# Optimization experiments

Hardware: AMD Instinct MI355X
Metric: run time of the kernel (lower is better)

Reference implementation:

```python
import jax, jax.numpy as jnp
import numpy as np

N = 20000      # nodes
E = 320000     # edges (avg degree 16)
D = 128        # emb_dim
L = 5          # num_layer
NV = 119       # node vocab (atom types)
EV = 5         # edge vocab (bond types)
BN_EPS = 1e-5


def setup_inputs() -> dict:
    key = jax.random.key(0)
    ks = jax.random.split(key, 8)
    s = 0.1
    return {
        "x": jax.random.randint(ks[0], (N,), 0, NV),
        "edge_index": jax.random.randint(ks[1], (2, E), 0, N),
        "edge_attr": jax.random.randint(ks[2], (E,), 0, EV),
        "node_emb1": jax.random.normal(ks[3], (NV, D), jnp.float32) * s,
        "node_emb2": jax.random.normal(ks[4], (NV, D), jnp.float32) * s,
        "edge_emb": jax.random.normal(ks[5], (2, L, EV, D), jnp.float32) * s,
        "eps": jnp.zeros((2, L), jnp.float32),
        "W": jax.random.normal(ks[6], (2, L, D, D), jnp.float32) / np.sqrt(D).astype(np.float32),
        "b": jnp.zeros((2, L, D), jnp.float32),
        "bn_gamma": jnp.ones((2, L, D), jnp.float32),
        "bn_beta": jnp.zeros((2, L, D), jnp.float32),
        "cross_unit": jnp.full((L, 2, 2), 0.5, jnp.float32),
    }


def gin_conv(h, src, dst, eattr, edge_tab, eps, W, b):
    # message: relu(x_j + edge_embedding), aggregated by add at target nodes
    msg = jax.nn.relu(h[src] + edge_tab[eattr])            # [E, D]
    agg = jax.ops.segment_sum(msg, dst, num_segments=h.shape[0])  # [N, D]
    return ((1.0 + eps) * h + agg) @ W.T + b               # mlp = single Linear


def batch_norm(h, gamma, beta):
    # training-mode BatchNorm1d over the node dimension (biased variance)
    mu = h.mean(axis=0)
    var = h.var(axis=0)
    return (h - mu) * jax.lax.rsqrt(var + BN_EPS) * gamma + beta


def reference(x, edge_index, edge_attr, node_emb1, node_emb2, edge_emb, eps, W, b,
              bn_gamma, bn_beta, cross_unit):
    src, dst = edge_index[0], edge_index[1]
    h1 = node_emb1[x]   # NodeEncoder tower 1
    h2 = node_emb2[x]   # NodeEncoder tower 2
    for l in range(L):
        a1 = gin_conv(h1, src, dst, edge_attr, edge_emb[0, l], eps[0, l], W[0, l], b[0, l])
        a1 = batch_norm(a1, bn_gamma[0, l], bn_beta[0, l])
        a2 = gin_conv(h2, src, dst, edge_attr, edge_emb[1, l], eps[1, l], W[1, l], b[1, l])
        a2 = batch_norm(a2, bn_gamma[1, l], bn_beta[1, l])
        if l < L - 1:
            a1 = jax.nn.relu(a1)
            a2 = jax.nn.relu(a2)
        # dropout: identity (eval mode / deterministic reference)
        # cross-stitch; note h_2 uses the UPDATED h_1 (faithful to source)
        c = cross_unit[l]
        n1 = c[0, 0] * a1 + c[0, 1] * a2
        n2 = c[1, 0] * n1 + c[1, 1] * a2
        h1, h2 = n1, n2
    return (h1, h2)  # JK == 'last'
```

## Files before the change

kernel.cpp:

```cpp
#include <hip/hip_runtime.h>

#define NN 20000
#define EE 320000
#define DD 128
#define LL 5
#define EVV 5
#define BNEPS 1e-5f
#define FB 313
#define EMB_BLOCKS 2500
#define CVT_BLOCKS 160
#define CNT_BLOCKS 1250

typedef __attribute__((ext_vector_type(8))) short bf8_t;
typedef __attribute__((ext_vector_type(4))) float f4_t;
typedef __attribute__((ext_vector_type(8))) unsigned short us8;

__device__ inline unsigned short f2bf(float f) {
    union { float f; unsigned u; } v;
    v.f = f;
    unsigned r = v.u + 0x7fffu + ((v.u >> 16) & 1u);
    return (unsigned short)(r >> 16);
}
__device__ inline float bf2f(unsigned short h) {
    union { unsigned u; float f; } v;
    v.u = ((unsigned)h) << 16;
    return v.f;
}
__device__ inline float4 bf2f4(ushort4 u) {
    float4 f;
    f.x = bf2f(u.x); f.y = bf2f(u.y); f.z = bf2f(u.z); f.w = bf2f(u.w);
    return f;
}
__device__ inline float4 add4(float4 a, float4 b) {
    float4 r;
    r.x = a.x + b.x; r.y = a.y + b.y; r.z = a.z + b.z; r.w = a.w + b.w;
    return r;
}

__device__ inline void xform4(float4 v1, float4 v2,
                              float4 s1, float4 t1, float4 s2, float4 t2,
                              float c00, float c01, float c10, float c11,
                              int dorelu, float4& n1, float4& n2) {
    float x1, x2, m1, m2;
#define XE(f)                                                    \
    x1 = v1.f * s1.f + t1.f;                                     \
    x2 = v2.f * s2.f + t2.f;                                     \
    x1 = dorelu ? fmaxf(x1, 0.f) : x1;                           \
    x2 = dorelu ? fmaxf(x2, 0.f) : x2;                           \
    m1 = c00 * x1 + c01 * x2;                                    \
    m2 = c10 * m1 + c11 * x2;                                    \
    n1.f = m1;                                                   \
    n2.f = m2;
    XE(x) XE(y) XE(z) XE(w)
#undef XE
}

__device__ inline void bn_coeffs(const float* __restrict__ statsL,
                                 const float* __restrict__ gall,
                                 const float* __restrict__ btall,
                                 int pl, int c,
                                 float4& s1, float4& t1, float4& s2, float4& t2) {
    const float inv = 1.0f / (float)NN;
    int ch = c * 4;
#define BNC(tw, sv, tv)                                                       \
    {                                                                         \
        const float* gp = gall + (size_t)((tw) * LL + pl) * DD + ch;          \
        const float* bp = btall + (size_t)((tw) * LL + pl) * DD + ch;         \
        float r[4];                                                           \
        _Pragma("unroll") for (int j = 0; j < 4; j++) {                       \
            float sum = statsL[(tw) * 256 + ch + j];                          \
            float sq = statsL[(tw) * 256 + 128 + ch + j];                     \
            float mu = sum * inv;                                             \
            float var = sq * inv - mu * mu;                                   \
            float rs = rsqrtf(var + BNEPS);                                   \
            float sc = rs * gp[j];                                            \
            r[j] = sc;                                                        \
            ((float*)&tv)[j] = bp[j] - mu * sc;                               \
        }                                                                     \
        sv.x = r[0]; sv.y = r[1]; sv.z = r[2]; sv.w = r[3];                   \
    }
    BNC(0, s1, t1)
    BNC(1, s2, t2)
#undef BNC
}

__device__ inline ushort4 hi4(float4 v) {
    ushort4 h;
    h.x = f2bf(v.x); h.y = f2bf(v.y); h.z = f2bf(v.z); h.w = f2bf(v.w);
    return h;
}
__device__ inline ushort4 lo4(float4 v, ushort4 h) {
    ushort4 l;
    l.x = f2bf(v.x - bf2f(h.x)); l.y = f2bf(v.y - bf2f(h.y));
    l.z = f2bf(v.z - bf2f(h.z)); l.w = f2bf(v.w - bf2f(h.w));
    return l;
}


__global__ __launch_bounds__(256) void prep_kernel(
    const int* __restrict__ x,
    const float4* __restrict__ e1, const float4* __restrict__ e2,
    ushort4* __restrict__ eh, ushort4* __restrict__ el,
    const float4* __restrict__ Wall,
    ushort4* __restrict__ Wbh, ushort4* __restrict__ Wbl,
    const int* __restrict__ dst, int* __restrict__ deg,
    float* __restrict__ stats,
    const float* __restrict__ etab, unsigned short* __restrict__ etb2) {
    int bid = blockIdx.x;
    int tid = threadIdx.x;
    if (bid < EMB_BLOCKS) {
        int idx = bid * 256 + tid;
        int r = idx >> 5, c = idx & 31;
        int v = x[r];
        float4 w1 = e1[v * 32 + c];
        float4 w2 = e2[v * 32 + c];
        ushort4 h = hi4(w1);
        eh[(size_t)r * 64 + c] = h;
        el[(size_t)r * 64 + c] = lo4(w1, h);
        h = hi4(w2);
        eh[(size_t)r * 64 + 32 + c] = h;
        el[(size_t)r * 64 + 32 + c] = lo4(w2, h);
    } else if (bid < EMB_BLOCKS + CVT_BLOCKS) {
        int i = (bid - EMB_BLOCKS) * 256 + tid;
        float4 w = Wall[i];
        ushort4 oh = hi4(w);
        Wbh[i] = oh;
        Wbl[i] = lo4(w, oh);
    } else if (bid < EMB_BLOCKS + CVT_BLOCKS + CNT_BLOCKS) {
        int e = (bid - EMB_BLOCKS - CVT_BLOCKS) * 256 + tid;
        atomicAdd(&deg[dst[e]], 1);
    } else {
#pragma unroll
        for (int i = 0; i < 10; i++) stats[i * 256 + tid] = 0.f;
        for (int idx = tid; idx < 2 * LL * EVV * DD; idx += 256) {
            int ch = idx & 127;
            int tw = (idx >> 7) & 1;
            int la = idx >> 8;
            int a = la % EVV;
            int l = la / EVV;
            etb2[idx] = f2bf(etab[((size_t)(tw * LL + l) * EVV + a) * DD + ch]);
        }
    }
}


__global__ __launch_bounds__(1024) void scan_kernel(const int* __restrict__ deg,
                                                    int* __restrict__ offs,
                                                    int* __restrict__ pos) {
    __shared__ int wsum[16];
    int t = threadIdx.x;
    int lane = t & 63, wv = t >> 6;
    int base = t * 20;
    int loc[20];
    int s = 0;
#pragma unroll
    for (int i = 0; i < 20; i++) {
        int j = base + i;
        int d = (j < NN) ? deg[j] : 0;
        loc[i] = d;
        s += d;
    }
    int incl = s;
#pragma unroll
    for (int o = 1; o < 64; o <<= 1) {
        int v = __shfl_up(incl, o, 64);
        if (lane >= o) incl += v;
    }
    if (lane == 63) wsum[wv] = incl;
    __syncthreads();
    if (t < 16) {
        int v = wsum[t];
        int iv = v;
#pragma unroll
        for (int o = 1; o < 16; o <<= 1) {
            int u = __shfl_up(iv, o, 64);
            if (t >= o) iv += u;
        }
        wsum[t] = iv - v;
    }
    __syncthreads();
    int run = wsum[wv] + (incl - s);
#pragma unroll
    for (int i = 0; i < 20; i++) {
        int j = base + i;
        if (j < NN) {
            offs[j] = run;
            pos[j] = run;
            run += loc[i];
        }
    }
}

__global__ __launch_bounds__(256) void scatter_kernel(const int* __restrict__ src,
                                                      const int* __restrict__ dst,
                                                      const int* __restrict__ eattr,
                                                      int* __restrict__ pos,
                                                      int2* __restrict__ erec) {
    int e = blockIdx.x * 256 + threadIdx.x;
    if (e < EE) {
        int d = dst[e];
        int p = atomicAdd(&pos[d], 1);
        erec[p] = make_int2(src[e], eattr[e]);
    }
}


__global__ __launch_bounds__(256) void xform_kernel(
    const ushort4* __restrict__ yh, const ushort4* __restrict__ yl,
    ushort4* __restrict__ hph, ushort4* __restrict__ hpl,
    const float* __restrict__ statsL,
    const float* __restrict__ gall, const float* __restrict__ btall,
    const float* __restrict__ crossp, int pl) {
    int idx = blockIdx.x * 256 + threadIdx.x;
    int r = idx >> 5, c = idx & 31;
    float4 s1, t1, s2, t2;
    bn_coeffs(statsL, gall, btall, pl, c, s1, t1, s2, t2);
    float c00 = crossp[0], c01 = crossp[1], c10 = crossp[2], c11 = crossp[3];
    float4 v1 = add4(bf2f4(yh[(size_t)r * 64 + c]), bf2f4(yl[(size_t)r * 64 + c]));
    float4 v2 = add4(bf2f4(yh[(size_t)r * 64 + 32 + c]), bf2f4(yl[(size_t)r * 64 + 32 + c]));
    float4 n1, n2;
    xform4(v1, v2, s1, t1, s2, t2, c00, c01, c10, c11, 1, n1, n2);
    ushort4 h = hi4(n1);
    hph[(size_t)r * 64 + c] = h;
    hpl[(size_t)r * 64 + c] = lo4(n1, h);
    h = hi4(n2);
    hph[(size_t)r * 64 + 32 + c] = h;
    hpl[(size_t)r * 64 + 32 + c] = lo4(n2, h);
}


__global__ __launch_bounds__(512, 4) void agg_gemm_kernel(
    const us8* __restrict__ hph, const us8* __restrict__ hpl,
    const us8* __restrict__ etb2, int layer,
    const int* __restrict__ offs, const int* __restrict__ deg,
    const int2* __restrict__ erec, const float* __restrict__ epsall,
    const unsigned short* __restrict__ Wbh, const unsigned short* __restrict__ Wbl,
    const float* __restrict__ ball,
    unsigned short* __restrict__ yh, unsigned short* __restrict__ yl,
    float* __restrict__ statsL) {
    __shared__ float accS[2 * 64 * 4 * 33];
    __shared__ float sP[2][2][4][DD];
    us8* uS = (us8*)accS;

    int tid = threadIdx.x;
    int w = tid >> 6, lane = tid & 63;

    {
        int slot = lane >> 5;
        int c = lane & 31;
        const us8* et = etb2 + (size_t)layer * EVV * 32;
        float ep = 1.0f + epsall[(c >> 4) * LL + layer];
#pragma unroll 1
        for (int rnd = 0; rnd < 8; rnd++) {
            int row = w * 8 + rnd;
            int node = blockIdx.x * 64 + row;
            us8 outv;
            if (node < NN) {
                int off = offs[node];
                int dg = deg[node];
                float a[8];
#pragma unroll
                for (int k = 0; k < 8; k++) a[k] = 0.f;
                int i = 0;
                for (; i + 8 <= dg; i += 8) {
                    int2 r0 = erec[off + i + slot];
                    int2 r1 = erec[off + i + 2 + slot];
                    int2 r2 = erec[off + i + 4 + slot];
                    int2 r3 = erec[off + i + 6 + slot];
                    us8 h0 = hph[(size_t)r0.x * 32 + c];
                    us8 h1 = hph[(size_t)r1.x * 32 + c];
                    us8 h2 = hph[(size_t)r2.x * 32 + c];
                    us8 h3 = hph[(size_t)r3.x * 32 + c];
                    us8 e0 = et[r0.y * 32 + c];
                    us8 e1 = et[r1.y * 32 + c];
                    us8 e2 = et[r2.y * 32 + c];
                    us8 e3 = et[r3.y * 32 + c];
#pragma unroll
                    for (int k = 0; k < 8; k++) {
                        a[k] += fmaxf(bf2f(h0[k]) + bf2f(e0[k]), 0.f);
                        a[k] += fmaxf(bf2f(h1[k]) + bf2f(e1[k]), 0.f);
                        a[k] += fmaxf(bf2f(h2[k]) + bf2f(e2[k]), 0.f);
                        a[k] += fmaxf(bf2f(h3[k]) + bf2f(e3[k]), 0.f);
                    }
                }
                for (; i < dg; i += 2) {
                    int j = i + slot;
                    bool valid = j < dg;
                    int e = off + (valid ? j : 0);
                    int2 r = erec[e];
                    us8 h = hph[(size_t)r.x * 32 + c];
                    us8 ev = et[r.y * 32 + c];
                    if (valid) {
#pragma unroll
                        for (int k = 0; k < 8; k++)
                            a[k] += fmaxf(bf2f(h[k]) + bf2f(ev[k]), 0.f);
                    }
                }
#pragma unroll
                for (int k = 0; k < 8; k++) a[k] += __shfl_xor(a[k], 32, 64);
                us8 sh = hph[(size_t)node * 32 + c];
                us8 sl = hpl[(size_t)node * 32 + c];
                us8 uh, ul;
#pragma unroll
                for (int k = 0; k < 8; k++) {
                    float u = ep * (bf2f(sh[k]) + bf2f(sl[k])) + a[k];
                    unsigned short h = f2bf(u);
                    uh[k] = h;
                    ul[k] = f2bf(u - bf2f(h));
                }
                outv = slot ? ul : uh;
            } else {
#pragma unroll
                for (int k = 0; k < 8; k++) outv[k] = 0;
            }
            int unit = slot * 32 + c;
            uS[row * 64 + (unit ^ (row & 7))] = outv;
        }
    }
    __syncthreads();

    int tower = w & 1, rt = w >> 1;
    int quad = lane >> 4, m = lane & 15;
    const bf8_t* Wh8 = (const bf8_t*)(Wbh + (size_t)(tower * LL + layer) * DD * DD);
    const bf8_t* Wl8 = (const bf8_t*)(Wbl + (size_t)(tower * LL + layer) * DD * DD);
    const float* bias = ball + (size_t)(tower * LL + layer) * DD;
    const bf8_t* u8 = (const bf8_t*)uS;

    f4_t acc[8];
#pragma unroll
    for (int nt = 0; nt < 8; nt++) {
        acc[nt][0] = 0.f; acc[nt][1] = 0.f; acc[nt][2] = 0.f; acc[nt][3] = 0.f;
    }
    int lrow = rt * 16 + m;
    int sw = lrow & 7;
#pragma unroll
    for (int kt = 0; kt < 4; kt++) {
        bf8_t ah = u8[lrow * 64 + ((tower * 16 + kt * 4 + quad) ^ sw)];
        bf8_t al = u8[lrow * 64 + ((tower * 16 + 32 + kt * 4 + quad) ^ sw)];
#pragma unroll
        for (int nt = 0; nt < 8; nt++) {
            bf8_t bh = Wh8[(nt * 16 + m) * 16 + kt * 4 + quad];
            bf8_t bl = Wl8[(nt * 16 + m) * 16 + kt * 4 + quad];
            acc[nt] = __builtin_amdgcn_mfma_f32_16x16x32_bf16(ah, bh, acc[nt], 0, 0, 0);
            acc[nt] = __builtin_amdgcn_mfma_f32_16x16x32_bf16(al, bh, acc[nt], 0, 0, 0);
            acc[nt] = __builtin_amdgcn_mfma_f32_16x16x32_bf16(ah, bl, acc[nt], 0, 0, 0);
        }
    }
    __syncthreads();

    float* aS = accS + tower * (64 * 4 * 33);
#pragma unroll
    for (int nt = 0; nt < 8; nt++) {
        int col = nt * 16 + m;
        float bv = bias[col];
        int cg = col >> 5, kk = col & 31;
        float s = 0.f, q = 0.f;
#pragma unroll
        for (int r = 0; r < 4; r++) {
            int lr2 = rt * 16 + quad * 4 + r;
            int row = blockIdx.x * 64 + lr2;
            float v = acc[nt][r] + bv;
            aS[(lr2 * 4 + cg) * 33 + kk] = v;
            if (row < NN) { s += v; q += v * v; }
        }
        s += __shfl_xor(s, 16, 64); s += __shfl_xor(s, 32, 64);
        q += __shfl_xor(q, 16, 64); q += __shfl_xor(q, 32, 64);
        if (quad == 0) {
            sP[tower][0][rt][col] = s;
            sP[tower][1][rt][col] = q;
        }
    }
    __syncthreads();

    {
        int lr = tid >> 3, g = tid & 7;
        int tw = g >> 2, cg = g & 3;
        int grow = blockIdx.x * 64 + lr;
        if (grow < NN) {
            const float* srcp = accS + tw * (64 * 4 * 33) + (lr * 4 + cg) * 33;
            us8* yhp = (us8*)yh;
            us8* ylp = (us8*)yl;
            size_t base = (size_t)grow * 32 + tw * 16 + cg * 4;
#pragma unroll
            for (int j = 0; j < 4; j++) {
                us8 hv, lv;
#pragma unroll
                for (int k = 0; k < 8; k++) {
                    float v = srcp[j * 8 + k];
                    unsigned short h = f2bf(v);
                    hv[k] = h;
                    lv[k] = f2bf(v - bf2f(h));
                }
                yhp[base + j] = hv;
                ylp[base + j] = lv;
            }
        }
    }

    {
        int tw = tid >> 8, idx = tid & 255;
        int sq = idx >> 7, ch = idx & 127;
        float v = sP[tw][sq][0][ch] + sP[tw][sq][1][ch] + sP[tw][sq][2][ch] + sP[tw][sq][3][ch];
        atomicAdd(&statsL[tw * 256 + idx], v);
    }
}


__global__ __launch_bounds__(256) void bn_final_kernel(
    const ushort4* __restrict__ yh, const ushort4* __restrict__ yl,
    float4* __restrict__ o1, float4* __restrict__ o2,
    const float* __restrict__ statsL,
    const float* __restrict__ gall, const float* __restrict__ btall,
    const float* __restrict__ crossp) {
    int idx = blockIdx.x * 256 + threadIdx.x;
    int r = idx >> 5, c = idx & 31;
    float4 s1, t1, s2, t2;
    bn_coeffs(statsL, gall, btall, LL - 1, c, s1, t1, s2, t2);
    float c00 = crossp[0], c01 = crossp[1], c10 = crossp[2], c11 = crossp[3];
    float4 v1 = add4(bf2f4(yh[(size_t)r * 64 + c]), bf2f4(yl[(size_t)r * 64 + c]));
    float4 v2 = add4(bf2f4(yh[(size_t)r * 64 + 32 + c]), bf2f4(yl[(size_t)r * 64 + 32 + c]));
    float4 n1, n2;
    xform4(v1, v2, s1, t1, s2, t2, c00, c01, c10, c11, 0, n1, n2);
    o1[(size_t)r * 32 + c] = n1;
    o2[(size_t)r * 32 + c] = n2;
}


extern "C" void kernel_launch(void* const* d_in, const int* in_sizes, int n_in,
                              void* d_out, int out_size, void* d_ws, size_t ws_size,
                              hipStream_t stream) {
    const int* x = (const int*)d_in[0];
    const int* eidx = (const int*)d_in[1];
    const int* eattr = (const int*)d_in[2];
    const float* emb1 = (const float*)d_in[3];
    const float* emb2 = (const float*)d_in[4];
    const float* etab = (const float*)d_in[5];
    const float* epsv = (const float*)d_in[6];
    const float* Wall = (const float*)d_in[7];
    const float* ball = (const float*)d_in[8];
    const float* gall = (const float*)d_in[9];
    const float* btall = (const float*)d_in[10];
    const float* cross = (const float*)d_in[11];
    float* out = (float*)d_out;

    const size_t ND = (size_t)NN * DD;
    char* p = (char*)d_ws;
    unsigned short* yh = (unsigned short*)p;   p += (size_t)NN * 256 * 2;
    unsigned short* yl = (unsigned short*)p;   p += (size_t)NN * 256 * 2;
    unsigned short* hph = (unsigned short*)p;  p += (size_t)NN * 256 * 2;
    unsigned short* hpl = (unsigned short*)p;  p += (size_t)NN * 256 * 2;
    unsigned short* eh = (unsigned short*)p;   p += (size_t)NN * 256 * 2;
    unsigned short* el = (unsigned short*)p;   p += (size_t)NN * 256 * 2;
    unsigned short* Wbh = (unsigned short*)p;  p += (size_t)2 * LL * DD * DD * 2;
    unsigned short* Wbl = (unsigned short*)p;  p += (size_t)2 * LL * DD * DD * 2;
    unsigned short* etb2 = (unsigned short*)p; p += (size_t)2 * LL * EVV * DD * 2;
    int* deg = (int*)p;               p += (size_t)NN * 4;
    int* offs = (int*)p;              p += (size_t)NN * 4;
    int* pos = (int*)p;               p += (size_t)NN * 4;
    int2* erec = (int2*)p;            p += (size_t)EE * 8;
    float* stats = (float*)p;         p += (size_t)LL * 512 * 4;

    const int* src = eidx;
    const int* dst = eidx + EE;

    hipMemsetAsync(deg, 0, (size_t)NN * 4, stream);
    prep_kernel<<<EMB_BLOCKS + CVT_BLOCKS + CNT_BLOCKS + 1, 256, 0, stream>>>(
        x, (const float4*)emb1, (const float4*)emb2,
        (ushort4*)eh, (ushort4*)el,
        (const float4*)Wall, (ushort4*)Wbh, (ushort4*)Wbl, dst, deg, stats,
        etab, etb2);
    scan_kernel<<<1, 1024, 0, stream>>>(deg, offs, pos);
    scatter_kernel<<<EE / 256, 256, 0, stream>>>(src, dst, eattr, pos, erec);

    for (int l = 0; l < LL; l++) {
        const unsigned short* hsrc_h = eh;
        const unsigned short* hsrc_l = el;
        if (l > 0) {
            xform_kernel<<<(NN * 32) / 256, 256, 0, stream>>>(
                (const ushort4*)yh, (const ushort4*)yl,
                (ushort4*)hph, (ushort4*)hpl,
                stats + (size_t)(l - 1) * 512, gall, btall,
                cross + (l - 1) * 4, l - 1);
            hsrc_h = hph;
            hsrc_l = hpl;
        }
        agg_gemm_kernel<<<FB, 512, 0, stream>>>(
            (const us8*)hsrc_h, (const us8*)hsrc_l, (const us8*)etb2, l,
            offs, deg, erec, epsv, Wbh, Wbl, ball, yh, yl,
            stats + (size_t)l * 512);
    }
    bn_final_kernel<<<(NN * 32) / 256, 256, 0, stream>>>(
        (const ushort4*)yh, (const ushort4*)yl, (float4*)out, (float4*)(out + ND),
        stats + (size_t)(LL - 1) * 512, gall, btall, cross + (LL - 1) * 4);
}
```

Baseline: 585.6 us.

## Split agg_gemm kernel across towers via second grid dimension

New measurement: 509.2 us. 13.0% less time.

```diff
diff --git a/kernel.cpp b/kernel.cpp
--- a/kernel.cpp
+++ b/kernel.cpp
@@ -229,7 +229,7 @@
 }
 
 
-__global__ __launch_bounds__(512, 4) void agg_gemm_kernel(
+__global__ __launch_bounds__(512, 8) void agg_gemm_kernel(
     const us8* __restrict__ hph, const us8* __restrict__ hpl,
     const us8* __restrict__ etb2, int layer,
     const int* __restrict__ offs, const int* __restrict__ deg,
@@ -238,23 +238,25 @@
     const float* __restrict__ ball,
     unsigned short* __restrict__ yh, unsigned short* __restrict__ yl,
     float* __restrict__ statsL) {
-    __shared__ float accS[2 * 64 * 4 * 33];
-    __shared__ float sP[2][2][4][DD];
+    __shared__ float accS[64 * 4 * 33];
+    __shared__ float sP[2][4][DD];
     us8* uS = (us8*)accS;
 
     int tid = threadIdx.x;
     int w = tid >> 6, lane = tid & 63;
+    int tower = blockIdx.y;
 
     {
-        int slot = lane >> 5;
-        int c = lane & 31;
+        int slot = lane >> 4;
+        int c = lane & 15;
+        int ubase = tower * 16 + c;
         const us8* et = etb2 + (size_t)layer * EVV * 32;
-        float ep = 1.0f + epsall[(c >> 4) * LL + layer];
+        float ep = 1.0f + epsall[tower * LL + layer];
 #pragma unroll 1
         for (int rnd = 0; rnd < 8; rnd++) {
             int row = w * 8 + rnd;
             int node = blockIdx.x * 64 + row;
-            us8 outv;
+            us8 uh, ul;
             if (node < NN) {
                 int off = offs[node];
                 int dg = deg[node];
@@ -264,32 +266,24 @@
                 int i = 0;
                 for (; i + 8 <= dg; i += 8) {
                     int2 r0 = erec[off + i + slot];
-                    int2 r1 = erec[off + i + 2 + slot];
-                    int2 r2 = erec[off + i + 4 + slot];
-                    int2 r3 = erec[off + i + 6 + slot];
-                    us8 h0 = hph[(size_t)r0.x * 32 + c];
-                    us8 h1 = hph[(size_t)r1.x * 32 + c];
-                    us8 h2 = hph[(size_t)r2.x * 32 + c];
-                    us8 h3 = hph[(size_t)r3.x * 32 + c];
-                    us8 e0 = et[r0.y * 32 + c];
-                    us8 e1 = et[r1.y * 32 + c];
-                    us8 e2 = et[r2.y * 32 + c];
-                    us8 e3 = et[r3.y * 32 + c];
+                    int2 r1 = erec[off + i + 4 + slot];
+                    us8 h0 = hph[(size_t)r0.x * 32 + ubase];
+                    us8 h1 = hph[(size_t)r1.x * 32 + ubase];
+                    us8 e0 = et[r0.y * 32 + ubase];
+                    us8 e1 = et[r1.y * 32 + ubase];
 #pragma unroll
                     for (int k = 0; k < 8; k++) {
                         a[k] += fmaxf(bf2f(h0[k]) + bf2f(e0[k]), 0.f);
                         a[k] += fmaxf(bf2f(h1[k]) + bf2f(e1[k]), 0.f);
-                        a[k] += fmaxf(bf2f(h2[k]) + bf2f(e2[k]), 0.f);
-                        a[k] += fmaxf(bf2f(h3[k]) + bf2f(e3[k]), 0.f);
                     }
                 }
-                for (; i < dg; i += 2) {
+                for (; i < dg; i += 4) {
                     int j = i + slot;
                     bool valid = j < dg;
                     int e = off + (valid ? j : 0);
                     int2 r = erec[e];
-                    us8 h = hph[(size_t)r.x * 32 + c];
-                    us8 ev = et[r.y * 32 + c];
+                    us8 h = hph[(size_t)r.x * 32 + ubase];
+                    us8 ev = et[r.y * 32 + ubase];
                     if (valid) {
 #pragma unroll
                         for (int k = 0; k < 8; k++)
@@ -297,10 +291,12 @@
                     }
                 }
 #pragma unroll
-                for (int k = 0; k < 8; k++) a[k] += __shfl_xor(a[k], 32, 64);
-                us8 sh = hph[(size_t)node * 32 + c];
-                us8 sl = hpl[(size_t)node * 32 + c];
-                us8 uh, ul;
+                for (int k = 0; k < 8; k++) {
+                    a[k] += __shfl_xor(a[k], 16, 64);
+                    a[k] += __shfl_xor(a[k], 32, 64);
+                }
+                us8 sh = hph[(size_t)node * 32 + ubase];
+                us8 sl = hpl[(size_t)node * 32 + ubase];
 #pragma unroll
                 for (int k = 0; k < 8; k++) {
                     float u = ep * (bf2f(sh[k]) + bf2f(sl[k])) + a[k];
@@ -308,50 +304,52 @@
                     uh[k] = h;
                     ul[k] = f2bf(u - bf2f(h));
                 }
-                outv = slot ? ul : uh;
             } else {
 #pragma unroll
-                for (int k = 0; k < 8; k++) outv[k] = 0;
+                for (int k = 0; k < 8; k++) { uh[k] = 0; ul[k] = 0; }
             }
-            int unit = slot * 32 + c;
-            uS[row * 64 + (unit ^ (row & 7))] = outv;
+            if (slot < 2) {
+                int unit = slot * 16 + c;
+                uS[row * 32 + (unit ^ (row & 7))] = slot ? ul : uh;
+            }
         }
     }
     __syncthreads();
 
-    int tower = w & 1, rt = w >> 1;
+    int rt = w >> 1, nh = w & 1;
     int quad = lane >> 4, m = lane & 15;
     const bf8_t* Wh8 = (const bf8_t*)(Wbh + (size_t)(tower * LL + layer) * DD * DD);
     const bf8_t* Wl8 = (const bf8_t*)(Wbl + (size_t)(tower * LL + layer) * DD * DD);
     const float* bias = ball + (size_t)(tower * LL + layer) * DD;
     const bf8_t* u8 = (const bf8_t*)uS;
 
-    f4_t acc[8];
-#pragma unroll
-    for (int nt = 0; nt < 8; nt++) {
+    f4_t acc[4];
+#pragma unroll
+    for (int nt = 0; nt < 4; nt++) {
         acc[nt][0] = 0.f; acc[nt][1] = 0.f; acc[nt][2] = 0.f; acc[nt][3] = 0.f;
     }
     int lrow = rt * 16 + m;
     int sw = lrow & 7;
 #pragma unroll
     for (int kt = 0; kt < 4; kt++) {
-        bf8_t ah = u8[lrow * 64 + ((tower * 16 + kt * 4 + quad) ^ sw)];
-        bf8_t al = u8[lrow * 64 + ((tower * 16 + 32 + kt * 4 + quad) ^ sw)];
-#pragma unroll
-        for (int nt = 0; nt < 8; nt++) {
+        int su = (kt * 4 + quad) ^ sw;
+        bf8_t ah = u8[lrow * 32 + su];
+        bf8_t al = u8[lrow * 32 + 16 + su];
+#pragma unroll
+        for (int ntl = 0; ntl < 4; ntl++) {
+            int nt = nh * 4 + ntl;
             bf8_t bh = Wh8[(nt * 16 + m) * 16 + kt * 4 + quad];
             bf8_t bl = Wl8[(nt * 16 + m) * 16 + kt * 4 + quad];
-            acc[nt] = __builtin_amdgcn_mfma_f32_16x16x32_bf16(ah, bh, acc[nt], 0, 0, 0);
-            acc[nt] = __builtin_amdgcn_mfma_f32_16x16x32_bf16(al, bh, acc[nt], 0, 0, 0);
-            acc[nt] = __builtin_amdgcn_mfma_f32_16x16x32_bf16(ah, bl, acc[nt], 0, 0, 0);
+            acc[ntl] = __builtin_amdgcn_mfma_f32_16x16x32_bf16(ah, bh, acc[ntl], 0, 0, 0);
+            acc[ntl] = __builtin_amdgcn_mfma_f32_16x16x32_bf16(al, bh, acc[ntl], 0, 0, 0);
+            acc[ntl] = __builtin_amdgcn_mfma_f32_16x16x32_bf16(ah, bl, acc[ntl], 0, 0, 0);
         }
     }
     __syncthreads();
 
-    float* aS = accS + tower * (64 * 4 * 33);
-#pragma unroll
-    for (int nt = 0; nt < 8; nt++) {
-        int col = nt * 16 + m;
+#pragma unroll
+    for (int ntl = 0; ntl < 4; ntl++) {
+        int col = (nh * 4 + ntl) * 16 + m;
         float bv = bias[col];
         int cg = col >> 5, kk = col & 31;
         float s = 0.f, q = 0.f;
@@ -359,34 +357,34 @@
         for (int r = 0; r < 4; r++) {
             int lr2 = rt * 16 + quad * 4 + r;
             int row = blockIdx.x * 64 + lr2;
-            float v = acc[nt][r] + bv;
-            aS[(lr2 * 4 + cg) * 33 + kk] = v;
+            float v = acc[ntl][r] + bv;
+            accS[(lr2 * 4 + cg) * 33 + kk] = v;
             if (row < NN) { s += v; q += v * v; }
         }
         s += __shfl_xor(s, 16, 64); s += __shfl_xor(s, 32, 64);
         q += __shfl_xor(q, 16, 64); q += __shfl_xor(q, 32, 64);
         if (quad == 0) {
-            sP[tower][0][rt][col] = s;
-            sP[tower][1][rt][col] = q;
+            sP[0][rt][col] = s;
+            sP[1][rt][col] = q;
         }
     }
     __syncthreads();
 
     {
         int lr = tid >> 3, g = tid & 7;
-        int tw = g >> 2, cg = g & 3;
+        int cg = g >> 1, jh = g & 1;
         int grow = blockIdx.x * 64 + lr;
         if (grow < NN) {
-            const float* srcp = accS + tw * (64 * 4 * 33) + (lr * 4 + cg) * 33;
+            const float* srcp = accS + (lr * 4 + cg) * 33;
             us8* yhp = (us8*)yh;
             us8* ylp = (us8*)yl;
-            size_t base = (size_t)grow * 32 + tw * 16 + cg * 4;
-#pragma unroll
-            for (int j = 0; j < 4; j++) {
+            size_t base = (size_t)grow * 32 + tower * 16 + cg * 4 + jh * 2;
+#pragma unroll
+            for (int j = 0; j < 2; j++) {
                 us8 hv, lv;
 #pragma unroll
                 for (int k = 0; k < 8; k++) {
-                    float v = srcp[j * 8 + k];
+                    float v = srcp[(jh * 2 + j) * 8 + k];
                     unsigned short h = f2bf(v);
                     hv[k] = h;
                     lv[k] = f2bf(v - bf2f(h));
@@ -397,11 +395,10 @@
         }
     }
 
-    {
-        int tw = tid >> 8, idx = tid & 255;
-        int sq = idx >> 7, ch = idx & 127;
-        float v = sP[tw][sq][0][ch] + sP[tw][sq][1][ch] + sP[tw][sq][2][ch] + sP[tw][sq][3][ch];
-        atomicAdd(&statsL[tw * 256 + idx], v);
+    if (tid < 256) {
+        int sq = tid >> 7, ch = tid & 127;
+        float v = sP[sq][0][ch] + sP[sq][1][ch] + sP[sq][2][ch] + sP[sq][3][ch];
+        atomicAdd(&statsL[tower * 256 + tid], v);
     }
 }
 
@@ -484,7 +481,7 @@
             hsrc_h = hph;
             hsrc_l = hpl;
         }
-        agg_gemm_kernel<<<FB, 512, 0, stream>>>(
+        agg_gemm_kernel<<<dim3(FB, 2), 512, 0, stream>>>(
             (const us8*)hsrc_h, (const us8*)hsrc_l, (const us8*)etb2, l,
             offs, deg, erec, epsv, Wbh, Wbl, ball, yh, yl,
             stats + (size_t)l * 512);
```

## Restructure agg_gemm to 16 nodes per 1024-thread block, one wave per node

Applied to the files above, without the earlier changes.

Measured after the change: 471.6 us, median of 3. 19.5% less time.

```diff
diff --git a/kernel.cpp b/kernel.cpp
--- a/kernel.cpp
+++ b/kernel.cpp
@@ -6,7 +6,7 @@
 #define LL 5
 #define EVV 5
 #define BNEPS 1e-5f
-#define FB 313
+#define FB 1250
 #define EMB_BLOCKS 2500
 #define CVT_BLOCKS 160
 #define CNT_BLOCKS 1250
@@ -229,7 +229,7 @@
 }
 
 
-__global__ __launch_bounds__(512, 4) void agg_gemm_kernel(
+__global__ __launch_bounds__(1024, 8) void agg_gemm_kernel(
     const us8* __restrict__ hph, const us8* __restrict__ hpl,
     const us8* __restrict__ etb2, int layer,
     const int* __restrict__ offs, const int* __restrict__ deg,
@@ -238,170 +238,149 @@
     const float* __restrict__ ball,
     unsigned short* __restrict__ yh, unsigned short* __restrict__ yl,
     float* __restrict__ statsL) {
-    __shared__ float accS[2 * 64 * 4 * 33];
-    __shared__ float sP[2][2][4][DD];
+    __shared__ float accS[16 * 8 * 33];
+    __shared__ float sP[2][2][DD];
     us8* uS = (us8*)accS;
 
     int tid = threadIdx.x;
     int w = tid >> 6, lane = tid & 63;
 
     {
+        int row = w;
+        int node = blockIdx.x * 16 + row;
         int slot = lane >> 5;
         int c = lane & 31;
         const us8* et = etb2 + (size_t)layer * EVV * 32;
         float ep = 1.0f + epsall[(c >> 4) * LL + layer];
-#pragma unroll 1
-        for (int rnd = 0; rnd < 8; rnd++) {
-            int row = w * 8 + rnd;
-            int node = blockIdx.x * 64 + row;
-            us8 outv;
-            if (node < NN) {
-                int off = offs[node];
-                int dg = deg[node];
-                float a[8];
-#pragma unroll
-                for (int k = 0; k < 8; k++) a[k] = 0.f;
-                int i = 0;
-                for (; i + 8 <= dg; i += 8) {
-                    int2 r0 = erec[off + i + slot];
-                    int2 r1 = erec[off + i + 2 + slot];
-                    int2 r2 = erec[off + i + 4 + slot];
-                    int2 r3 = erec[off + i + 6 + slot];
-                    us8 h0 = hph[(size_t)r0.x * 32 + c];
-                    us8 h1 = hph[(size_t)r1.x * 32 + c];
-                    us8 h2 = hph[(size_t)r2.x * 32 + c];
-                    us8 h3 = hph[(size_t)r3.x * 32 + c];
-                    us8 e0 = et[r0.y * 32 + c];
-                    us8 e1 = et[r1.y * 32 + c];
-                    us8 e2 = et[r2.y * 32 + c];
-                    us8 e3 = et[r3.y * 32 + c];
-#pragma unroll
-                    for (int k = 0; k < 8; k++) {
-                        a[k] += fmaxf(bf2f(h0[k]) + bf2f(e0[k]), 0.f);
-                        a[k] += fmaxf(bf2f(h1[k]) + bf2f(e1[k]), 0.f);
-                        a[k] += fmaxf(bf2f(h2[k]) + bf2f(e2[k]), 0.f);
-                        a[k] += fmaxf(bf2f(h3[k]) + bf2f(e3[k]), 0.f);
-                    }
-                }
-                for (; i < dg; i += 2) {
-                    int j = i + slot;
-                    bool valid = j < dg;
-                    int e = off + (valid ? j : 0);
-                    int2 r = erec[e];
-                    us8 h = hph[(size_t)r.x * 32 + c];
-                    us8 ev = et[r.y * 32 + c];
-                    if (valid) {
-#pragma unroll
-                        for (int k = 0; k < 8; k++)
-                            a[k] += fmaxf(bf2f(h[k]) + bf2f(ev[k]), 0.f);
-                    }
-                }
-#pragma unroll
-                for (int k = 0; k < 8; k++) a[k] += __shfl_xor(a[k], 32, 64);
-                us8 sh = hph[(size_t)node * 32 + c];
-                us8 sl = hpl[(size_t)node * 32 + c];
-                us8 uh, ul;
-#pragma unroll
-                for (int k = 0; k < 8; k++) {
-                    float u = ep * (bf2f(sh[k]) + bf2f(sl[k])) + a[k];
-                    unsigned short h = f2bf(u);
-                    uh[k] = h;
-                    ul[k] = f2bf(u - bf2f(h));
-                }
-                outv = slot ? ul : uh;
-            } else {
-#pragma unroll
-                for (int k = 0; k < 8; k++) outv[k] = 0;
+
+        int off = offs[node];
+        int dg = deg[node];
+        float a[8];
+#pragma unroll
+        for (int k = 0; k < 8; k++) a[k] = 0.f;
+        int i = 0;
+        for (; i + 8 <= dg; i += 8) {
+            int2 r0 = erec[off + i + slot];
+            int2 r1 = erec[off + i + 2 + slot];
+            int2 r2 = erec[off + i + 4 + slot];
+            int2 r3 = erec[off + i + 6 + slot];
+            us8 h0 = hph[(size_t)r0.x * 32 + c];
+            us8 h1 = hph[(size_t)r1.x * 32 + c];
+            us8 h2 = hph[(size_t)r2.x * 32 + c];
+            us8 h3 = hph[(size_t)r3.x * 32 + c];
+            us8 e0 = et[r0.y * 32 + c];
+            us8 e1 = et[r1.y * 32 + c];
+            us8 e2 = et[r2.y * 32 + c];
+            us8 e3 = et[r3.y * 32 + c];
+#pragma unroll
+            for (int k = 0; k < 8; k++) {
+                a[k] += fmaxf(bf2f(h0[k]) + bf2f(e0[k]), 0.f);
+                a[k] += fmaxf(bf2f(h1[k]) + bf2f(e1[k]), 0.f);
+                a[k] += fmaxf(bf2f(h2[k]) + bf2f(e2[k]), 0.f);
+                a[k] += fmaxf(bf2f(h3[k]) + bf2f(e3[k]), 0.f);
             }
-            int unit = slot * 32 + c;
-            uS[row * 64 + (unit ^ (row & 7))] = outv;
-        }
+        }
+        for (; i < dg; i += 2) {
+            int j = i + slot;
+            bool valid = j < dg;
+            int e = off + (valid ? j : 0);
+            int2 r = erec[e];
+            us8 h = hph[(size_t)r.x * 32 + c];
+            us8 ev = et[r.y * 32 + c];
+            if (valid) {
+#pragma unroll
+                for (int k = 0; k < 8; k++) a[k] += fmaxf(bf2f(h[k]) + bf2f(ev[k]), 0.f);
+            }
+        }
+#pragma unroll
+        for (int k = 0; k < 8; k++) a[k] += __shfl_xor(a[k], 32, 64);
+
+        us8 sh = hph[(size_t)node * 32 + c];
+        us8 sl = hpl[(size_t)node * 32 + c];
+        us8 uh, ul;
+#pragma unroll
+        for (int k = 0; k < 8; k++) {
+            float u = ep * (bf2f(sh[k]) + bf2f(sl[k])) + a[k];
+            unsigned short h = f2bf(u);
+            uh[k] = h;
+            ul[k] = f2bf(u - bf2f(h));
+        }
+        int unit = slot * 32 + c;
+        uS[row * 64 + (unit ^ (row & 7))] = slot ? ul : uh;
     }
     __syncthreads();
 
-    int tower = w & 1, rt = w >> 1;
+    int tw = w >> 3, nt = w & 7;
     int quad = lane >> 4, m = lane & 15;
-    const bf8_t* Wh8 = (const bf8_t*)(Wbh + (size_t)(tower * LL + layer) * DD * DD);
-    const bf8_t* Wl8 = (const bf8_t*)(Wbl + (size_t)(tower * LL + layer) * DD * DD);
-    const float* bias = ball + (size_t)(tower * LL + layer) * DD;
+    const bf8_t* Wh8 = (const bf8_t*)(Wbh + (size_t)(tw * LL + layer) * DD * DD);
+    const bf8_t* Wl8 = (const bf8_t*)(Wbl + (size_t)(tw * LL + layer) * DD * DD);
+    const float* bias = ball + (size_t)(tw * LL + layer) * DD;
     const bf8_t* u8 = (const bf8_t*)uS;
 
-    f4_t acc[8];
-#pragma unroll
-    for (int nt = 0; nt < 8; nt++) {
-        acc[nt][0] = 0.f; acc[nt][1] = 0.f; acc[nt][2] = 0.f; acc[nt][3] = 0.f;
-    }
-    int lrow = rt * 16 + m;
+    f4_t acc;
+    acc[0] = 0.f; acc[1] = 0.f; acc[2] = 0.f; acc[3] = 0.f;
+    int lrow = m;
     int sw = lrow & 7;
 #pragma unroll
     for (int kt = 0; kt < 4; kt++) {
-        bf8_t ah = u8[lrow * 64 + ((tower * 16 + kt * 4 + quad) ^ sw)];
-        bf8_t al = u8[lrow * 64 + ((tower * 16 + 32 + kt * 4 + quad) ^ sw)];
-#pragma unroll
-        for (int nt = 0; nt < 8; nt++) {
-            bf8_t bh = Wh8[(nt * 16 + m) * 16 + kt * 4 + quad];
-            bf8_t bl = Wl8[(nt * 16 + m) * 16 + kt * 4 + quad];
-            acc[nt] = __builtin_amdgcn_mfma_f32_16x16x32_bf16(ah, bh, acc[nt], 0, 0, 0);
-            acc[nt] = __builtin_amdgcn_mfma_f32_16x16x32_bf16(al, bh, acc[nt], 0, 0, 0);
-            acc[nt] = __builtin_amdgcn_mfma_f32_16x16x32_bf16(ah, bl, acc[nt], 0, 0, 0);
-        }
+        int x = kt * 4 + quad;
+        bf8_t ah = u8[lrow * 64 + (tw * 16 + (x ^ sw))];
+        bf8_t al = u8[lrow * 64 + (32 + tw * 16 + (x ^ sw))];
+        bf8_t bh = Wh8[(nt * 16 + m) * 16 + x];
+        bf8_t bl = Wl8[(nt * 16 + m) * 16 + x];
+        acc = __builtin_amdgcn_mfma_f32_16x16x32_bf16(ah, bh, acc, 0, 0, 0);
+        acc = __builtin_amdgcn_mfma_f32_16x16x32_bf16(al, bh, acc, 0, 0, 0);
+        acc = __builtin_amdgcn_mfma_f32_16x16x32_bf16(ah, bl, acc, 0, 0, 0);
     }
     __syncthreads();
 
-    float* aS = accS + tower * (64 * 4 * 33);
-#pragma unroll
-    for (int nt = 0; nt < 8; nt++) {
+    {
         int col = nt * 16 + m;
         float bv = bias[col];
-        int cg = col >> 5, kk = col & 31;
+        int gc = tw * 128 + col;
+        int cg = gc >> 5, kk = gc & 31;
         float s = 0.f, q = 0.f;
 #pragma unroll
         for (int r = 0; r < 4; r++) {
-            int lr2 = rt * 16 + quad * 4 + r;
-            int row = blockIdx.x * 64 + lr2;
-            float v = acc[nt][r] + bv;
-            aS[(lr2 * 4 + cg) * 33 + kk] = v;
-            if (row < NN) { s += v; q += v * v; }
+            int lr2 = quad * 4 + r;
+            float v = acc[r] + bv;
+            accS[(lr2 * 8 + cg) * 33 + kk] = v;
+            s += v; q += v * v;
         }
         s += __shfl_xor(s, 16, 64); s += __shfl_xor(s, 32, 64);
         q += __shfl_xor(q, 16, 64); q += __shfl_xor(q, 32, 64);
         if (quad == 0) {
-            sP[tower][0][rt][col] = s;
-            sP[tower][1][rt][col] = q;
+            sP[tw][0][col] = s;
+            sP[tw][1][col] = q;
         }
     }
     __syncthreads();
 
     {
-        int lr = tid >> 3, g = tid & 7;
-        int tw = g >> 2, cg = g & 3;
-        int grow = blockIdx.x * 64 + lr;
-        if (grow < NN) {
-            const float* srcp = accS + tw * (64 * 4 * 33) + (lr * 4 + cg) * 33;
-            us8* yhp = (us8*)yh;
-            us8* ylp = (us8*)yl;
-            size_t base = (size_t)grow * 32 + tw * 16 + cg * 4;
-#pragma unroll
-            for (int j = 0; j < 4; j++) {
-                us8 hv, lv;
-#pragma unroll
-                for (int k = 0; k < 8; k++) {
-                    float v = srcp[j * 8 + k];
-                    unsigned short h = f2bf(v);
-                    hv[k] = h;
-                    lv[k] = f2bf(v - bf2f(h));
-                }
-                yhp[base + j] = hv;
-                ylp[base + j] = lv;
+        int t = tid & 511;
+        int row = t >> 5, unit = t & 31;
+        int grow = blockIdx.x * 16 + row;
+        int cg = unit >> 2, kb = (unit & 3) * 8;
+        const float* srcp = accS + (row * 8 + cg) * 33 + kb;
+        us8 v8;
+        if (tid < 512) {
+#pragma unroll
+            for (int k = 0; k < 8; k++) v8[k] = f2bf(srcp[k]);
+            ((us8*)yh)[(size_t)grow * 32 + unit] = v8;
+        } else {
+#pragma unroll
+            for (int k = 0; k < 8; k++) {
+                float v = srcp[k];
+                v8[k] = f2bf(v - bf2f(f2bf(v)));
             }
-        }
-    }
-
-    {
-        int tw = tid >> 8, idx = tid & 255;
+            ((us8*)yl)[(size_t)grow * 32 + unit] = v8;
+        }
+    }
+
+    if (tid < 512) {
+        int twi = tid >> 8, idx = tid & 255;
         int sq = idx >> 7, ch = idx & 127;
-        float v = sP[tw][sq][0][ch] + sP[tw][sq][1][ch] + sP[tw][sq][2][ch] + sP[tw][sq][3][ch];
-        atomicAdd(&statsL[tw * 256 + idx], v);
+        atomicAdd(&statsL[twi * 256 + idx], sP[twi][sq][ch]);
     }
 }
 
@@ -484,7 +463,7 @@
             hsrc_h = hph;
             hsrc_l = hpl;
         }
-        agg_gemm_kernel<<<FB, 512, 0, stream>>>(
+        agg_gemm_kernel<<<FB, 1024, 0, stream>>>(
             (const us8*)hsrc_h, (const us8*)hsrc_l, (const us8*)etb2, l,
             offs, deg, erec, epsv, Wbh, Wbl, ball, yh, yl,
             stats + (size_t)l * 512);
```
